# Kernel tuning notes

Measured on AMD Instinct MI355X. Metric: run time of the kernel, lower is better.

The kernel has to match this reference:

```python
import jax, jax.numpy as jnp
import numpy as np

D_MODEL = 1024
D_FF = 4096
EPS = 1e-5


def layer_norm(x, gamma, beta):
    mu = jnp.mean(x, axis=-1, keepdims=True)
    var = jnp.var(x, axis=-1, keepdims=True)
    return (x - mu) * jax.lax.rsqrt(var + EPS) * gamma + beta


def attention(x_q, x_kv, WQ, WK, WV, causal):
    Q = x_q @ WQ          # [B,Sq,D]
    K = x_kv @ WK         # [B,Sk,D]
    V = x_kv @ WV
    scale = 1.0 / jnp.sqrt(jnp.asarray(Q.shape[-1], Q.dtype))
    scores = jnp.einsum('bqd,bkd->bqk', Q, K) * scale
    if causal:
        Sq, Sk = scores.shape[-2], scores.shape[-1]
        mask = jnp.triu(jnp.full((Sq, Sk), -jnp.inf, scores.dtype), k=1)
        scores = scores + mask
    attn = jax.nn.softmax(scores, axis=-1)
    return jnp.einsum('bqk,bkd->bqd', attn, V)


def setup_inputs() -> dict:
    key = jax.random.key(0)
    ks = jax.random.split(key, 16)
    B, S = 4, 2048
    s = 0.02
    inp = {
        'y': jax.random.normal(ks[0], (B, S, D_MODEL), jnp.float32),
        'Z': jax.random.normal(ks[1], (B, S, D_MODEL), jnp.float32),
        'WQ1': jax.random.normal(ks[2], (D_MODEL, D_MODEL), jnp.float32) * s,
        'WK1': jax.random.normal(ks[3], (D_MODEL, D_MODEL), jnp.float32) * s,
        'WV1': jax.random.normal(ks[4], (D_MODEL, D_MODEL), jnp.float32) * s,
        'WQ2': jax.random.normal(ks[5], (D_MODEL, D_MODEL), jnp.float32) * s,
        'WK2': jax.random.normal(ks[6], (D_MODEL, D_MODEL), jnp.float32) * s,
        'WV2': jax.random.normal(ks[7], (D_MODEL, D_MODEL), jnp.float32) * s,
        'W_ff1': jax.random.normal(ks[8], (D_MODEL, D_FF), jnp.float32) * s,
        'b_ff1': jnp.zeros((D_FF,), jnp.float32),
        'W_ff2': jax.random.normal(ks[9], (D_FF, D_MODEL), jnp.float32) * s,
        'b_ff2': jnp.zeros((D_MODEL,), jnp.float32),
        'g1': jnp.ones((D_MODEL,), jnp.float32), 'be1': jnp.zeros((D_MODEL,), jnp.float32),
        'g2': jnp.ones((D_MODEL,), jnp.float32), 'be2': jnp.zeros((D_MODEL,), jnp.float32),
        'g3': jnp.ones((D_MODEL,), jnp.float32), 'be3': jnp.zeros((D_MODEL,), jnp.float32),
    }
    return inp


def reference(y, Z, WQ1, WK1, WV1, WQ2, WK2, WV2, W_ff1, b_ff1, W_ff2, b_ff2,
              g1, be1, g2, be2, g3, be3):
    # masked self-attention + add&norm
    y = layer_norm(y + attention(y, y, WQ1, WK1, WV1, causal=True), g1, be1)
    # cross-attention + add&norm
    y = layer_norm(y + attention(y, Z, WQ2, WK2, WV2, causal=False), g2, be2)
    # FFN + add&norm
    h = jax.nn.relu(y @ W_ff1 + b_ff1) @ W_ff2 + b_ff2
    y = layer_norm(y + h, g3, be3)
    return y
```

## Files before the change

### kernel.cpp

```cpp
#include <hip/hip_runtime.h>
#include <cstddef>

typedef unsigned short u16;
typedef __attribute__((ext_vector_type(8))) short bf16x8;
typedef __attribute__((ext_vector_type(4))) float f32x4;

__device__ __forceinline__ u16 f2bf(float f) {
  union { float f; unsigned u; } x; x.f = f;
  unsigned r = x.u + 0x7fffu + ((x.u >> 16) & 1u);
  return (u16)(r >> 16);
}
__device__ __forceinline__ float bf2f(u16 h) {
  union { unsigned u; float f; } x; x.u = ((unsigned)h) << 16;
  return x.f;
}

__device__ __forceinline__ void gll16(const u16* g, u16* ldsbase) {
  __builtin_amdgcn_global_load_lds(
      (const __attribute__((address_space(1))) void*)g,
      (__attribute__((address_space(3))) void*)ldsbase, 16, 0, 0);
}

__global__ __launch_bounds__(256) void f32_to_bf16(const float* __restrict__ in,
                                                   u16* __restrict__ out, size_t n) {
  size_t i = (size_t)blockIdx.x * 256 + threadIdx.x;
  if (i < n) out[i] = f2bf(in[i]);
}

__global__ __launch_bounds__(256) void transpose_f32_bf16(const float* __restrict__ in,
                                                          u16* __restrict__ out,
                                                          int R, int C) {
  __shared__ float tile[32][33];
  int c0 = blockIdx.x * 32, r0 = blockIdx.y * 32;
  int tx = threadIdx.x & 31, ty = threadIdx.x >> 5;
  #pragma unroll
  for (int i = ty; i < 32; i += 8)
    tile[i][tx] = in[(size_t)(r0 + i) * C + c0 + tx];
  __syncthreads();
  #pragma unroll
  for (int i = ty; i < 32; i += 8)
    out[(size_t)(c0 + i) * R + r0 + tx] = f2bf(tile[tx][i]);
}

enum { EPI_F32 = 0, EPI_BF16 = 1, EPI_BF16_SCALE = 2,
       EPI_BIAS_RELU_BF16 = 3, EPI_BIAS_F32 = 4 };
enum { MODE_FULL = 0, MODE_TRI = 1, MODE_CAUSAL_K = 2 };

template <int EPI, int MODE, int BM, int BN>
__global__ __launch_bounds__(512) void gemm256(
    const u16* __restrict__ A, const u16* __restrict__ Bt,
    void* __restrict__ C0, const float* __restrict__ bias,
    const u16* __restrict__ A2, const u16* __restrict__ B2, int dsplit,
    int K, int lda, int ldb, int ldc,
    long long sA, long long sB, long long sC)
{
  constexpr int WM  = BM / 128;
  constexpr int WN  = 8 / WM;
  constexpr int CPW = BN / WN;
  constexpr int NF  = CPW / 16;
  constexpr int nBr = BN / 64;
  constexpr int nAr = BM / 64;
  constexpr int NBUF = (BM == 256 && BN == 256) ? 2 : 3;

  __shared__ __align__(16) u16 lA[NBUF][BM * 64];
  __shared__ __align__(16) u16 lB[NBUF][BN * 64];

  const unsigned gx = gridDim.x, gxy = gridDim.x * gridDim.y;
  unsigned id = blockIdx.x + gx * blockIdx.y + gxy * blockIdx.z;
  const unsigned nb = gxy * gridDim.z;
  unsigned p = id;
  if ((nb & 7u) == 0u) p = (id & 7u) * (nb >> 3) + (id >> 3);
  int z, mi, ni;
  if constexpr (MODE == MODE_TRI) {
    z = (int)(p / gxy);
    int r = (int)(p % gxy);
    int m = 0;
    if constexpr (BN == 256) {
      while ((m + 1) * (m + 2) / 2 <= r) m++;
      mi = m; ni = r - m * (m + 1) / 2;
    } else {
      while ((m + 1) * (m + 2) <= r) m++;
      mi = m; ni = r - m * (m + 1);
    }
  } else {
    z = (int)(p / gxy);
    const unsigned rem = p % gxy;
    mi = (int)(rem / gx);
    ni = (int)(rem % gx);
  }
  if (dsplit && ni >= dsplit) {
    A = A2; Bt = B2;
    C0 = (void*)((u16*)C0 + (size_t)dsplit * BN);
    ni -= dsplit;
  }
  const int m0 = mi * BM, n0 = ni * BN;

  A  += (long long)z * sA;
  Bt += (long long)z * sB;

  int NT = K >> 6;
  if constexpr (MODE == MODE_CAUSAL_K) NT = (m0 + BM) >> 6;

  const int t    = threadIdx.x;
  const int lane = t & 63;
  const int wave = t >> 6;
  const int wr   = (WM == 1) ? 0 : (wave >> 2);
  const int wc   = (WM == 1) ? wave : (wave & 3);
  const int quad = lane >> 4;
  const int lrow = lane & 15;

  const int srow = lane >> 3;
  const int scol = ((lane & 7) ^ srow) * 8;
  const u16* gAp = A  + (size_t)(m0 + wave * 8 + srow) * lda + scol;
  const u16* gBp = Bt + (size_t)(n0 + wave * 8 + srow) * ldb + scol;
  const size_t a64 = (size_t)64 * lda, b64 = (size_t)64 * ldb;
  const int lw = wave * 512;

  const int pg0 = (quad ^ (lrow & 7)) * 8;
  const int pg1 = pg0 ^ 32;
  const int rA = (wr * 128 + lrow) * 64;
  const int rB = (wc * CPW + lrow) * 64;

  f32x4 acc[8][NF];
  const f32x4 zero = {0.f, 0.f, 0.f, 0.f};
  #pragma unroll
  for (int i = 0; i < 8; i++)
    #pragma unroll
    for (int j = 0; j < NF; j++) acc[i][j] = zero;

  bf16x8 X[4][2];
  bf16x8 Y[4][2];
  bf16x8 bfr[NF][2];

  auto rdX = [&](const u16* s) {
    #pragma unroll
    for (int mf = 0; mf < 4; ++mf) {
      X[mf][0] = *(const bf16x8*)(s + rA + mf * 1024 + pg0);
      X[mf][1] = *(const bf16x8*)(s + rA + mf * 1024 + pg1);
    }
  };
  auto rdY = [&](const u16* s) {
    #pragma unroll
    for (int mf = 0; mf < 4; ++mf) {
      Y[mf][0] = *(const bf16x8*)(s + rA + (mf + 4) * 1024 + pg0);
      Y[mf][1] = *(const bf16x8*)(s + rA + (mf + 4) * 1024 + pg1);
    }
  };
  auto rdB = [&](const u16* s) {
    #pragma unroll
    for (int nf = 0; nf < NF; ++nf) {
      bfr[nf][0] = *(const bf16x8*)(s + rB + nf * 1024 + pg0);
      bfr[nf][1] = *(const bf16x8*)(s + rB + nf * 1024 + pg1);
    }
  };

  if constexpr (NBUF == 2) {
    auto stageB2 = [&](int b, int kt) {
      const int k = kt * 64;
      gll16(gBp + k,           &lB[b][lw]);
      gll16(gBp + k + b64,     &lB[b][4096 + lw]);
      gll16(gBp + k + 2 * b64, &lB[b][8192 + lw]);
      gll16(gBp + k + 3 * b64, &lB[b][12288 + lw]);
    };
    auto stageA2 = [&](int b, int kt) {
      const int k = kt * 64;
      gll16(gAp + k,           &lA[b][lw]);
      gll16(gAp + k + a64,     &lA[b][4096 + lw]);
      gll16(gAp + k + 2 * a64, &lA[b][8192 + lw]);
      gll16(gAp + k + 3 * a64, &lA[b][12288 + lw]);
    };

    stageB2(0, 0); stageA2(0, 0);
    if (NT > 1) {
      stageB2(1, 1);
      asm volatile("s_waitcnt vmcnt(4)" ::: "memory");
    } else {
      asm volatile("s_waitcnt vmcnt(0)" ::: "memory");
    }
    __builtin_amdgcn_s_barrier();

    for (int kt = 0; kt < NT; ++kt) {
      const int bsel = kt & 1;
      const u16* sa = &lA[bsel][0];
      const u16* sb = &lB[bsel][0];

      rdX(sa); rdB(sb);
      if (kt + 1 < NT) stageA2(bsel ^ 1, kt + 1);
      asm volatile("s_waitcnt lgkmcnt(0)" ::: "memory");
      __builtin_amdgcn_sched_barrier(0);
      __builtin_amdgcn_s_setprio(1);
      #pragma unroll
      for (int mf = 0; mf < 4; ++mf)
        #pragma unroll
        for (int nf = 0; nf < 4; ++nf) {
          acc[mf][nf] = __builtin_amdgcn_mfma_f32_16x16x32_bf16(bfr[nf][0], X[mf][0], acc[mf][nf], 0, 0, 0);
          acc[mf][nf] = __builtin_amdgcn_mfma_f32_16x16x32_bf16(bfr[nf][1], X[mf][1], acc[mf][nf], 0, 0, 0);
        }
      __builtin_amdgcn_s_setprio(0);
      __builtin_amdgcn_s_barrier();

      rdY(sa);
      if (kt + 2 < NT) stageB2(bsel, kt + 2);
      asm volatile("s_waitcnt lgkmcnt(0)" ::: "memory");
      __builtin_amdgcn_sched_barrier(0);
      __builtin_amdgcn_s_setprio(1);
      #pragma unroll
      for (int mf = 0; mf < 4; ++mf)
        #pragma unroll
        for (int nf = 0; nf < 4; ++nf) {
          acc[mf + 4][nf] = __builtin_amdgcn_mfma_f32_16x16x32_bf16(bfr[nf][0], Y[mf][0], acc[mf + 4][nf], 0, 0, 0);
          acc[mf + 4][nf] = __builtin_amdgcn_mfma_f32_16x16x32_bf16(bfr[nf][1], Y[mf][1], acc[mf + 4][nf], 0, 0, 0);
        }
      __builtin_amdgcn_s_setprio(0);
      if (kt + 2 < NT)      asm volatile("s_waitcnt vmcnt(4)" ::: "memory");
      else if (kt + 1 < NT) asm volatile("s_waitcnt vmcnt(0)" ::: "memory");
      __builtin_amdgcn_s_barrier();
    }
  } else {
    u16 *a0 = &lA[0][0], *a1 = &lA[1][0], *a2 = &lA[2][0];
    u16 *b0 = &lB[0][0], *b1 = &lB[1][0], *b2 = &lB[2][0];
    auto stage6 = [&](u16* ba, u16* bb, int kt) {
      const int k = kt * 64;
      #pragma unroll
      for (int s = 0; s < nBr; ++s)
        gll16(gBp + k + (size_t)s * b64, bb + s * 4096 + lw);
      #pragma unroll
      for (int s = 0; s < nAr; ++s)
        gll16(gAp + k + (size_t)s * a64, ba + s * 4096 + lw);
    };

    stage6(a0, b0, 0);
    if (NT > 1) {
      stage6(a1, b1, 1);
      asm volatile("s_waitcnt vmcnt(6)" ::: "memory");
    } else {
      asm volatile("s_waitcnt vmcnt(0)" ::: "memory");
    }
    __builtin_amdgcn_s_barrier();

    for (int kt = 0; kt < NT; ++kt) {
      rdX(a0); rdY(a0); rdB(b0);
      if (kt + 2 < NT) stage6(a2, b2, kt + 2);
      asm volatile("s_waitcnt lgkmcnt(0)" ::: "memory");
      __builtin_amdgcn_sched_barrier(0);
      __builtin_amdgcn_s_setprio(1);
      #pragma unroll
      for (int mf = 0; mf < 4; ++mf)
        #pragma unroll
        for (int nf = 0; nf < 2; ++nf) {
          acc[mf][nf] = __builtin_amdgcn_mfma_f32_16x16x32_bf16(bfr[nf][0], X[mf][0], acc[mf][nf], 0, 0, 0);
          acc[mf][nf] = __builtin_amdgcn_mfma_f32_16x16x32_bf16(bfr[nf][1], X[mf][1], acc[mf][nf], 0, 0, 0);
        }
      #pragma unroll
      for (int mf = 0; mf < 4; ++mf)
        #pragma unroll
        for (int nf = 0; nf < 2; ++nf) {
          acc[mf + 4][nf] = __builtin_amdgcn_mfma_f32_16x16x32_bf16(bfr[nf][0], Y[mf][0], acc[mf + 4][nf], 0, 0, 0);
          acc[mf + 4][nf] = __builtin_amdgcn_mfma_f32_16x16x32_bf16(bfr[nf][1], Y[mf][1], acc[mf + 4][nf], 0, 0, 0);
        }
      __builtin_amdgcn_s_setprio(0);
      if (kt + 2 < NT)      asm volatile("s_waitcnt vmcnt(6)" ::: "memory");
      else if (kt + 1 < NT) asm volatile("s_waitcnt vmcnt(0)" ::: "memory");
      __builtin_amdgcn_s_barrier();
      u16* tp;
      tp = a0; a0 = a1; a1 = a2; a2 = tp;
      tp = b0; b0 = b1; b1 = b2; b2 = tp;
    }
  }

  const size_t zoff = (size_t)((long long)z * sC);
  #pragma unroll
  for (int mf = 0; mf < 8; ++mf) {
    #pragma unroll
    for (int nf = 0; nf < NF; ++nf) {
      const size_t m  = (size_t)(m0 + wr * 128 + mf * 16 + lrow);
      const size_t nc = (size_t)(n0 + wc * CPW + nf * 16 + quad * 4);
      const size_t idx = zoff + m * (size_t)ldc + nc;
      f32x4 v = acc[mf][nf];
      if constexpr (EPI == EPI_F32) {
        *(float4*)((float*)C0 + idx) = make_float4(v[0], v[1], v[2], v[3]);
      } else if constexpr (EPI == EPI_BF16) {
        ushort4 o; o.x = f2bf(v[0]); o.y = f2bf(v[1]); o.z = f2bf(v[2]); o.w = f2bf(v[3]);
        *(ushort4*)((u16*)C0 + idx) = o;
      } else if constexpr (EPI == EPI_BF16_SCALE) {
        ushort4 o;
        o.x = f2bf(v[0] * 0.03125f); o.y = f2bf(v[1] * 0.03125f);
        o.z = f2bf(v[2] * 0.03125f); o.w = f2bf(v[3] * 0.03125f);
        *(ushort4*)((u16*)C0 + idx) = o;
      } else if constexpr (EPI == EPI_BIAS_RELU_BF16) {
        const float4 bb = *(const float4*)(bias + nc);
        float y0 = v[0] + bb.x, y1 = v[1] + bb.y, y2 = v[2] + bb.z, y3 = v[3] + bb.w;
        ushort4 o;
        o.x = f2bf(y0 > 0.f ? y0 : 0.f); o.y = f2bf(y1 > 0.f ? y1 : 0.f);
        o.z = f2bf(y2 > 0.f ? y2 : 0.f); o.w = f2bf(y3 > 0.f ? y3 : 0.f);
        *(ushort4*)((u16*)C0 + idx) = o;
      } else {
        const float4 bb = *(const float4*)(bias + nc);
        *(float4*)((float*)C0 + idx) =
            make_float4(v[0] + bb.x, v[1] + bb.y, v[2] + bb.z, v[3] + bb.w);
      }
    }
  }
}

__global__ __launch_bounds__(256) void softmax_bf16(u16* __restrict__ SP, int causal) {
  __shared__ float red[8];
  const int row = blockIdx.x;
  const int q = row & 2047;
  u16* p = SP + (size_t)row * 2048;
  const int t = threadIdx.x;
  const int base = t * 8;
  const int limit  = causal ? (q + 1) : 2048;
  const int wlimit = causal ? (((q >> 8) + 1) << 8) : 2048;

  float v[8];
  if (base < limit) {
    uint4 raw = *(const uint4*)(p + base);
    unsigned w[4] = {raw.x, raw.y, raw.z, raw.w};
    #pragma unroll
    for (int j = 0; j < 4; j++) {
      union { unsigned u; float f; } lo, hi;
      lo.u = w[j] << 16; hi.u = w[j] & 0xffff0000u;
      v[2 * j] = lo.f; v[2 * j + 1] = hi.f;
    }
    #pragma unroll
    for (int j = 0; j < 8; j++) if (base + j >= limit) v[j] = -3.4e38f;
  } else {
    #pragma unroll
    for (int j = 0; j < 8; j++) v[j] = -3.4e38f;
  }

  float mx = v[0];
  #pragma unroll
  for (int j = 1; j < 8; j++) mx = fmaxf(mx, v[j]);
  #pragma unroll
  for (int o = 32; o > 0; o >>= 1) mx = fmaxf(mx, __shfl_down(mx, o));
  if ((t & 63) == 0) red[t >> 6] = mx;
  __syncthreads();
  mx = fmaxf(fmaxf(red[0], red[1]), fmaxf(red[2], red[3]));

  float s = 0.f;
  #pragma unroll
  for (int j = 0; j < 8; j++) { float e = __expf(v[j] - mx); v[j] = e; s += e; }
  #pragma unroll
  for (int o = 32; o > 0; o >>= 1) s += __shfl_down(s, o);
  if ((t & 63) == 0) red[4 + (t >> 6)] = s;
  __syncthreads();
  const float inv = 1.f / (red[4] + red[5] + red[6] + red[7]);

  if (base < wlimit) {
    unsigned o4[4];
    #pragma unroll
    for (int j = 0; j < 4; j++)
      o4[j] = (unsigned)f2bf(v[2 * j] * inv) | ((unsigned)f2bf(v[2 * j + 1] * inv) << 16);
    *(uint4*)(p + base) = make_uint4(o4[0], o4[1], o4[2], o4[3]);
  }
}

template <int ABF>
__global__ __launch_bounds__(256) void ln_residual(const void* __restrict__ a_,
                                                   const float* __restrict__ b,
                                                   const float* __restrict__ g,
                                                   const float* __restrict__ be,
                                                   float* __restrict__ outf,
                                                   u16* __restrict__ outb) {
  __shared__ float red[8];
  const size_t base = (size_t)blockIdx.x * 1024;
  const int t = threadIdx.x;
  const int i0 = t * 4;

  float va[4];
  if constexpr (ABF) {
    const ushort4 h = *(const ushort4*)((const u16*)a_ + base + i0);
    va[0] = bf2f(h.x); va[1] = bf2f(h.y); va[2] = bf2f(h.z); va[3] = bf2f(h.w);
  } else {
    const float4 f = *(const float4*)((const float*)a_ + base + i0);
    va[0] = f.x; va[1] = f.y; va[2] = f.z; va[3] = f.w;
  }
  const float4 vb = *(const float4*)(b + base + i0);
  float v[4] = {va[0] + vb.x, va[1] + vb.y, va[2] + vb.z, va[3] + vb.w};

  float s = v[0] + v[1] + v[2] + v[3];
  #pragma unroll
  for (int o = 32; o > 0; o >>= 1) s += __shfl_down(s, o);
  if ((t & 63) == 0) red[t >> 6] = s;
  __syncthreads();
  const float mean = (red[0] + red[1] + red[2] + red[3]) * (1.f / 1024.f);

  float qq = 0.f;
  #pragma unroll
  for (int i = 0; i < 4; i++) { float d = v[i] - mean; qq += d * d; }
  #pragma unroll
  for (int o = 32; o > 0; o >>= 1) qq += __shfl_down(qq, o);
  if ((t & 63) == 0) red[4 + (t >> 6)] = qq;
  __syncthreads();
  const float rstd = rsqrtf((red[4] + red[5] + red[6] + red[7]) * (1.f / 1024.f) + 1e-5f);

  const float4 gg = *(const float4*)(g + i0);
  const float4 bb = *(const float4*)(be + i0);
  float y0 = (v[0] - mean) * rstd * gg.x + bb.x;
  float y1 = (v[1] - mean) * rstd * gg.y + bb.y;
  float y2 = (v[2] - mean) * rstd * gg.z + bb.z;
  float y3 = (v[3] - mean) * rstd * gg.w + bb.w;
  if (outf) *(float4*)(outf + base + i0) = make_float4(y0, y1, y2, y3);
  if (outb) {
    ushort4 o4; o4.x = f2bf(y0); o4.y = f2bf(y1); o4.z = f2bf(y2); o4.w = f2bf(y3);
    *(ushort4*)(outb + base + i0) = o4;
  }
}

extern "C" void kernel_launch(void* const* d_in, const int* in_sizes, int n_in,
                              void* d_out, int out_size, void* d_ws, size_t ws_size,
                              hipStream_t stream)
{
  const float* y_in = (const float*)d_in[0];
  const float* Z_in = (const float*)d_in[1];
  const float* WQ1  = (const float*)d_in[2];
  const float* WK1  = (const float*)d_in[3];
  const float* WV1  = (const float*)d_in[4];
  const float* WQ2  = (const float*)d_in[5];
  const float* WK2  = (const float*)d_in[6];
  const float* WV2  = (const float*)d_in[7];
  const float* Wff1 = (const float*)d_in[8];
  const float* bff1 = (const float*)d_in[9];
  const float* Wff2 = (const float*)d_in[10];
  const float* bff2 = (const float*)d_in[11];
  const float* g1  = (const float*)d_in[12];
  const float* be1 = (const float*)d_in[13];
  const float* g2  = (const float*)d_in[14];
  const float* be2 = (const float*)d_in[15];
  const float* g3  = (const float*)d_in[16];
  const float* be3 = (const float*)d_in[17];
  (void)in_sizes; (void)n_in; (void)out_size;

  constexpr int Bn = 4, S = 2048, D = 1024, DF = 4096;
  constexpr long long BS = (long long)Bn * S;
  const long long SD = (long long)S * D;
  const long long SS = (long long)S * S;
  const long long SD2 = (long long)S * 2 * D;

  char* ws = (char*)d_ws;
  size_t off = 0;
  auto alloc = [&](size_t bytes) -> char* {
    char* p = ws + off;
    off += (bytes + 255) & ~(size_t)255;
    return p;
  };

  u16* wq1t  = (u16*)alloc((size_t)D * D * 2);
  u16* wk1t  = (u16*)alloc((size_t)D * D * 2);
  u16* wv1t  = (u16*)alloc((size_t)D * D * 2);
  u16* wq2t  = (u16*)alloc((size_t)D * D * 2);
  u16* wk2t  = (u16*)alloc((size_t)D * D * 2);
  u16* wv2t  = (u16*)alloc((size_t)D * D * 2);
  u16* wff1t = (u16*)alloc((size_t)D * DF * 2);
  u16* wff2t = (u16*)alloc((size_t)D * DF * 2);
  u16* ybf   = (u16*)alloc((size_t)BS * D * 2);
  u16* zbf   = (u16*)alloc((size_t)BS * D * 2);
  u16* QKb   = (u16*)alloc((size_t)BS * 2 * D * 2);
  u16* Vtb   = (u16*)alloc((size_t)D * BS * 2);
  u16* SPb   = (u16*)alloc((size_t)Bn * S * S * 2);
  float* attnF = (float*)alloc((size_t)BS * D * 4);
  u16*   y1b = ybf;
  u16*   y2b = zbf;
  u16*   Hb  = QKb;
  float* Fb  = attnF;

  if (off > ws_size) return;

  const dim3 blk(256);
  const dim3 blk512(512);

  f32_to_bf16<<<dim3((unsigned)((BS * D) / 256)), blk, 0, stream>>>(y_in, ybf, (size_t)BS * D);
  f32_to_bf16<<<dim3((unsigned)((BS * D) / 256)), blk, 0, stream>>>(Z_in, zbf, (size_t)BS * D);
  transpose_f32_bf16<<<dim3(D / 32, D / 32), blk, 0, stream>>>(WQ1, wq1t, D, D);
  transpose_f32_bf16<<<dim3(D / 32, D / 32), blk, 0, stream>>>(WK1, wk1t, D, D);
  transpose_f32_bf16<<<dim3(D / 32, D / 32), blk, 0, stream>>>(WV1, wv1t, D, D);
  transpose_f32_bf16<<<dim3(D / 32, D / 32), blk, 0, stream>>>(WQ2, wq2t, D, D);
  transpose_f32_bf16<<<dim3(D / 32, D / 32), blk, 0, stream>>>(WK2, wk2t, D, D);
  transpose_f32_bf16<<<dim3(D / 32, D / 32), blk, 0, stream>>>(WV2, wv2t, D, D);
  transpose_f32_bf16<<<dim3(DF / 32, D / 32), blk, 0, stream>>>(Wff1, wff1t, D, DF);
  transpose_f32_bf16<<<dim3(D / 32, DF / 32), blk, 0, stream>>>(Wff2, wff2t, DF, D);

  gemm256<EPI_BF16, MODE_FULL, 256, 256><<<dim3(2 * D / 256, BS / 256, 1), blk512, 0, stream>>>(
      ybf, wq1t, QKb, nullptr, nullptr, nullptr, 0, D, D, D, 2 * D, 0, 0, 0);
  gemm256<EPI_BF16, MODE_FULL, 128, 256><<<dim3((unsigned)(BS / 256), D / 128, 1), blk512, 0, stream>>>(
      wv1t, ybf, Vtb, nullptr, nullptr, nullptr, 0, D, D, D, (int)BS, 0, 0, 0);
  gemm256<EPI_BF16_SCALE, MODE_TRI, 256, 128><<<dim3(72, 1, Bn), blk512, 0, stream>>>(
      QKb, QKb + D, SPb, nullptr, nullptr, nullptr, 0, D, 2 * D, 2 * D, S, SD2, SD2, SS);
  softmax_bf16<<<dim3((unsigned)(Bn * S)), blk, 0, stream>>>(SPb, 1);
  gemm256<EPI_F32, MODE_CAUSAL_K, 256, 128><<<dim3(D / 128, S / 256, Bn), blk512, 0, stream>>>(
      SPb, Vtb, attnF, nullptr, nullptr, nullptr, 0, S, S, (int)BS, D, SS, S, SD);
  ln_residual<0><<<dim3((unsigned)BS), blk, 0, stream>>>(y_in, attnF, g1, be1, nullptr, y1b);

  gemm256<EPI_BF16, MODE_FULL, 256, 128><<<dim3(2 * D / 128, BS / 256, 1), blk512, 0, stream>>>(
      y1b, wq2t, QKb, nullptr, zbf, wk2t, 8, D, D, D, 2 * D, 0, 0, 0);
  gemm256<EPI_BF16, MODE_FULL, 128, 256><<<dim3((unsigned)(BS / 256), D / 128, 1), blk512, 0, stream>>>(
      wv2t, zbf, Vtb, nullptr, nullptr, nullptr, 0, D, D, D, (int)BS, 0, 0, 0);
  gemm256<EPI_BF16_SCALE, MODE_FULL, 256, 256><<<dim3(S / 256, S / 256, Bn), blk512, 0, stream>>>(
      QKb, QKb + D, SPb, nullptr, nullptr, nullptr, 0, D, 2 * D, 2 * D, S, SD2, SD2, SS);
  softmax_bf16<<<dim3((unsigned)(Bn * S)), blk, 0, stream>>>(SPb, 0);
  gemm256<EPI_F32, MODE_FULL, 256, 128><<<dim3(D / 128, S / 256, Bn), blk512, 0, stream>>>(
      SPb, Vtb, attnF, nullptr, nullptr, nullptr, 0, S, S, (int)BS, D, SS, S, SD);
  ln_residual<1><<<dim3((unsigned)BS), blk, 0, stream>>>(y1b, attnF, g2, be2, nullptr, y2b);

  gemm256<EPI_BIAS_RELU_BF16, MODE_FULL, 256, 256><<<dim3(DF / 256, BS / 256, 1), blk512, 0, stream>>>(
      y2b, wff1t, Hb, bff1, nullptr, nullptr, 0, D, D, D, DF, 0, 0, 0);
  gemm256<EPI_BIAS_F32, MODE_FULL, 256, 128><<<dim3(D / 128, BS / 256, 1), blk512, 0, stream>>>(
      Hb, wff2t, Fb, bff2, nullptr, nullptr, 0, DF, DF, DF, D, 0, 0, 0);
  ln_residual<1><<<dim3((unsigned)BS), blk, 0, stream>>>(y2b, Fb, g3, be3, (float*)d_out, nullptr);
}
```

Measured before the change: 712.9 us.

## Software-pipeline LDS fragment reads with double-buffered registers in GEMM main loop

Restructures both GEMM main loops so the LDS-to-register fragment reads for the next k-tile are issued before the MFMAs of the current tile. Fragments are held in ping-pong register sets (even and odd), and the loop is unrolled by two. Partial lgkmcnt waits replace the full drains, so LDS read latency overlaps matrix-core work. This raises register pressure from the doubled fragment sets, which could cause spills. The new waitcnt and barrier ordering also carries correctness risk.

New measurement: 1.156 ms. 1.62x slower.

```diff
diff --git a/kernel.cpp b/kernel.cpp
--- a/kernel.cpp
+++ b/kernel.cpp
@@ -45,6 +45,93 @@
 enum { EPI_F32 = 0, EPI_BF16 = 1, EPI_BF16_SCALE = 2,
        EPI_BIAS_RELU_BF16 = 3, EPI_BIAS_F32 = 4 };
 enum { MODE_FULL = 0, MODE_TRI = 1, MODE_CAUSAL_K = 2 };
+
+#define RDX(SET, s)                                                           \
+  {                                                                           \
+    _Pragma("unroll")                                                         \
+    for (int mf = 0; mf < 4; ++mf) {                                          \
+      SET[mf][0] = *(const bf16x8*)((s) + rA + mf * 1024 + pg0);              \
+      SET[mf][1] = *(const bf16x8*)((s) + rA + mf * 1024 + pg1);              \
+    }                                                                         \
+  }
+#define RDY(SET, s)                                                           \
+  {                                                                           \
+    _Pragma("unroll")                                                         \
+    for (int mf = 0; mf < 4; ++mf) {                                          \
+      SET[mf][0] = *(const bf16x8*)((s) + rA + (mf + 4) * 1024 + pg0);        \
+      SET[mf][1] = *(const bf16x8*)((s) + rA + (mf + 4) * 1024 + pg1);        \
+    }                                                                         \
+  }
+#define RDBN(SET, s)                                                          \
+  {                                                                           \
+    _Pragma("unroll")                                                         \
+    for (int nf = 0; nf < NF; ++nf) {                                         \
+      SET[nf][0] = *(const bf16x8*)((s) + rB + nf * 1024 + pg0);              \
+      SET[nf][1] = *(const bf16x8*)((s) + rB + nf * 1024 + pg1);              \
+    }                                                                         \
+  }
+#define MMQ(MO, AF, BF)                                                       \
+  {                                                                           \
+    _Pragma("unroll")                                                         \
+    for (int mf = 0; mf < 4; ++mf) {                                          \
+      _Pragma("unroll")                                                       \
+      for (int nf = 0; nf < NF; ++nf) {                                       \
+        acc[mf + MO][nf] = __builtin_amdgcn_mfma_f32_16x16x32_bf16(           \
+            BF[nf][0], AF[mf][0], acc[mf + MO][nf], 0, 0, 0);                 \
+        acc[mf + MO][nf] = __builtin_amdgcn_mfma_f32_16x16x32_bf16(           \
+            BF[nf][1], AF[mf][1], acc[mf + MO][nf], 0, 0, 0);                 \
+      }                                                                       \
+    }                                                                         \
+  }
+
+#define T256(kt, BC, BN_)                                                     \
+  {                                                                           \
+    const int bsel = (kt) & 1;                                                \
+    const u16* sa  = &lA[bsel][0];                                            \
+    const u16* sa1 = &lA[bsel ^ 1][0];                                        \
+    const u16* sb1 = &lB[bsel ^ 1][0];                                        \
+            \
+    RDY(Y, sa);                                                               \
+    if ((kt) + 1 < NT) stageA2(bsel ^ 1, (kt) + 1);                           \
+    __builtin_amdgcn_sched_barrier(0);                                        \
+    asm volatile("s_waitcnt lgkmcnt(8)" ::: "memory");                        \
+    __builtin_amdgcn_sched_barrier(0);                                        \
+    __builtin_amdgcn_s_setprio(1);                                            \
+    MMQ(0, X, BC);                                                            \
+    __builtin_amdgcn_s_setprio(0);                                            \
+    if ((kt) + 1 < NT) asm volatile("s_waitcnt vmcnt(0)" ::: "memory");       \
+    __builtin_amdgcn_s_barrier();                                             \
+        \
+    if ((kt) + 1 < NT) { RDX(X, sa1); RDBN(BN_, sb1); }                       \
+    if ((kt) + 2 < NT) stageB2(bsel, (kt) + 2);                               \
+    __builtin_amdgcn_sched_barrier(0);                                        \
+    if ((kt) + 1 < NT) asm volatile("s_waitcnt lgkmcnt(15)" ::: "memory");    \
+    else               asm volatile("s_waitcnt lgkmcnt(0)" ::: "memory");     \
+    __builtin_amdgcn_sched_barrier(0);                                        \
+    __builtin_amdgcn_s_setprio(1);                                            \
+    MMQ(4, Y, BC);                                                            \
+    __builtin_amdgcn_s_setprio(0);                                            \
+    __builtin_amdgcn_s_barrier();                                             \
+  }
+
+#define TNAR(kt, XC, YC, BC, XN, YN, BN_)                                     \
+  {                                                                           \
+    if ((kt) + 2 < NT) stage6(a2, b2, (kt) + 2);                              \
+    if ((kt) + 1 < NT) { RDX(XN, a1); RDY(YN, a1); RDBN(BN_, b1); }           \
+    __builtin_amdgcn_sched_barrier(0);                                        \
+    if ((kt) + 1 < NT) asm volatile("s_waitcnt lgkmcnt(15)" ::: "memory");    \
+    else               asm volatile("s_waitcnt lgkmcnt(0)" ::: "memory");     \
+    __builtin_amdgcn_sched_barrier(0);                                        \
+    __builtin_amdgcn_s_setprio(1);                                            \
+    MMQ(0, XC, BC);                                                           \
+    MMQ(4, YC, BC);                                                           \
+    __builtin_amdgcn_s_setprio(0);                                            \
+    if ((kt) + 1 < NT) asm volatile("s_waitcnt vmcnt(0)" ::: "memory");       \
+    __builtin_amdgcn_s_barrier();                                             \
+    u16* tp_;                                                                 \
+    tp_ = a0; a0 = a1; a1 = a2; a2 = tp_;                                     \
+    tp_ = b0; b0 = b1; b1 = b2; b2 = tp_;                                     \
+  }
 
 template <int EPI, int MODE, int BM, int BN>
 __global__ __launch_bounds__(512) void gemm256(
@@ -128,33 +215,10 @@
     #pragma unroll
     for (int j = 0; j < NF; j++) acc[i][j] = zero;
 
-  bf16x8 X[4][2];
-  bf16x8 Y[4][2];
-  bf16x8 bfr[NF][2];
-
-  auto rdX = [&](const u16* s) {
-    #pragma unroll
-    for (int mf = 0; mf < 4; ++mf) {
-      X[mf][0] = *(const bf16x8*)(s + rA + mf * 1024 + pg0);
-      X[mf][1] = *(const bf16x8*)(s + rA + mf * 1024 + pg1);
-    }
-  };
-  auto rdY = [&](const u16* s) {
-    #pragma unroll
-    for (int mf = 0; mf < 4; ++mf) {
-      Y[mf][0] = *(const bf16x8*)(s + rA + (mf + 4) * 1024 + pg0);
-      Y[mf][1] = *(const bf16x8*)(s + rA + (mf + 4) * 1024 + pg1);
-    }
-  };
-  auto rdB = [&](const u16* s) {
-    #pragma unroll
-    for (int nf = 0; nf < NF; ++nf) {
-      bfr[nf][0] = *(const bf16x8*)(s + rB + nf * 1024 + pg0);
-      bfr[nf][1] = *(const bf16x8*)(s + rB + nf * 1024 + pg1);
-    }
-  };
-
   if constexpr (NBUF == 2) {
+    bf16x8 X[4][2], Y[4][2];
+    bf16x8 BE[NF][2], BO[NF][2];
+
     auto stageB2 = [&](int b, int kt) {
       const int k = kt * 64;
       gll16(gBp + k,           &lB[b][lw]);
@@ -178,45 +242,16 @@
       asm volatile("s_waitcnt vmcnt(0)" ::: "memory");
     }
     __builtin_amdgcn_s_barrier();
-
-    for (int kt = 0; kt < NT; ++kt) {
-      const int bsel = kt & 1;
-      const u16* sa = &lA[bsel][0];
-      const u16* sb = &lB[bsel][0];
-
-      rdX(sa); rdB(sb);
-      if (kt + 1 < NT) stageA2(bsel ^ 1, kt + 1);
-      asm volatile("s_waitcnt lgkmcnt(0)" ::: "memory");
-      __builtin_amdgcn_sched_barrier(0);
-      __builtin_amdgcn_s_setprio(1);
-      #pragma unroll
-      for (int mf = 0; mf < 4; ++mf)
-        #pragma unroll
-        for (int nf = 0; nf < 4; ++nf) {
-          acc[mf][nf] = __builtin_amdgcn_mfma_f32_16x16x32_bf16(bfr[nf][0], X[mf][0], acc[mf][nf], 0, 0, 0);
-          acc[mf][nf] = __builtin_amdgcn_mfma_f32_16x16x32_bf16(bfr[nf][1], X[mf][1], acc[mf][nf], 0, 0, 0);
-        }
-      __builtin_amdgcn_s_setprio(0);
-      __builtin_amdgcn_s_barrier();
-
-      rdY(sa);
-      if (kt + 2 < NT) stageB2(bsel, kt + 2);
-      asm volatile("s_waitcnt lgkmcnt(0)" ::: "memory");
-      __builtin_amdgcn_sched_barrier(0);
-      __builtin_amdgcn_s_setprio(1);
-      #pragma unroll
-      for (int mf = 0; mf < 4; ++mf)
-        #pragma unroll
-        for (int nf = 0; nf < 4; ++nf) {
-          acc[mf + 4][nf] = __builtin_amdgcn_mfma_f32_16x16x32_bf16(bfr[nf][0], Y[mf][0], acc[mf + 4][nf], 0, 0, 0);
-          acc[mf + 4][nf] = __builtin_amdgcn_mfma_f32_16x16x32_bf16(bfr[nf][1], Y[mf][1], acc[mf + 4][nf], 0, 0, 0);
-        }
-      __builtin_amdgcn_s_setprio(0);
-      if (kt + 2 < NT)      asm volatile("s_waitcnt vmcnt(4)" ::: "memory");
-      else if (kt + 1 < NT) asm volatile("s_waitcnt vmcnt(0)" ::: "memory");
-      __builtin_amdgcn_s_barrier();
+    RDX(X, &lA[0][0]);
+    RDBN(BE, &lB[0][0]);
+
+    for (int kt = 0; kt < NT; kt += 2) {
+      T256(kt, BE, BO);
+      if (kt + 1 < NT) T256(kt + 1, BO, BE);
     }
   } else {
+    bf16x8 XE[4][2], YE[4][2], XO[4][2], YO[4][2];
+    bf16x8 BE[NF][2], BO[NF][2];
     u16 *a0 = &lA[0][0], *a1 = &lA[1][0], *a2 = &lA[2][0];
     u16 *b0 = &lB[0][0], *b1 = &lB[1][0], *b2 = &lB[2][0];
     auto stage6 = [&](u16* ba, u16* bb, int kt) {
@@ -230,41 +265,14 @@
     };
 
     stage6(a0, b0, 0);
-    if (NT > 1) {
-      stage6(a1, b1, 1);
-      asm volatile("s_waitcnt vmcnt(6)" ::: "memory");
-    } else {
-      asm volatile("s_waitcnt vmcnt(0)" ::: "memory");
-    }
+    if (NT > 1) stage6(a1, b1, 1);
+    asm volatile("s_waitcnt vmcnt(0)" ::: "memory");
     __builtin_amdgcn_s_barrier();
-
-    for (int kt = 0; kt < NT; ++kt) {
-      rdX(a0); rdY(a0); rdB(b0);
-      if (kt + 2 < NT) stage6(a2, b2, kt + 2);
-      asm volatile("s_waitcnt lgkmcnt(0)" ::: "memory");
-      __builtin_amdgcn_sched_barrier(0);
-      __builtin_amdgcn_s_setprio(1);
-      #pragma unroll
-      for (int mf = 0; mf < 4; ++mf)
-        #pragma unroll
-        for (int nf = 0; nf < 2; ++nf) {
-          acc[mf][nf] = __builtin_amdgcn_mfma_f32_16x16x32_bf16(bfr[nf][0], X[mf][0], acc[mf][nf], 0, 0, 0);
-          acc[mf][nf] = __builtin_amdgcn_mfma_f32_16x16x32_bf16(bfr[nf][1], X[mf][1], acc[mf][nf], 0, 0, 0);
-        }
-      #pragma unroll
-      for (int mf = 0; mf < 4; ++mf)
-        #pragma unroll
-        for (int nf = 0; nf < 2; ++nf) {
-          acc[mf + 4][nf] = __builtin_amdgcn_mfma_f32_16x16x32_bf16(bfr[nf][0], Y[mf][0], acc[mf + 4][nf], 0, 0, 0);
-          acc[mf + 4][nf] = __builtin_amdgcn_mfma_f32_16x16x32_bf16(bfr[nf][1], Y[mf][1], acc[mf + 4][nf], 0, 0, 0);
-        }
-      __builtin_amdgcn_s_setprio(0);
-      if (kt + 2 < NT)      asm volatile("s_waitcnt vmcnt(6)" ::: "memory");
-      else if (kt + 1 < NT) asm volatile("s_waitcnt vmcnt(0)" ::: "memory");
-      __builtin_amdgcn_s_barrier();
-      u16* tp;
-      tp = a0; a0 = a1; a1 = a2; a2 = tp;
-      tp = b0; b0 = b1; b1 = b2; b2 = tp;
+    RDX(XE, a0); RDY(YE, a0); RDBN(BE, b0);
+
+    for (int kt = 0; kt < NT; kt += 2) {
+      TNAR(kt, XE, YE, BE, XO, YO, BO);
+      if (kt + 1 < NT) TNAR(kt + 1, XO, YO, BO, XE, YE, BE);
     }
   }
 
@@ -303,6 +311,13 @@
   }
 }
 
+#undef T256
+#undef TNAR
+#undef MMQ
+#undef RDX
+#undef RDY
+#undef RDBN
+
 __global__ __launch_bounds__(256) void softmax_bf16(u16* __restrict__ SP, int causal) {
   __shared__ float red[8];
   const int row = blockIdx.x;
```

## Interleave LDS reads, global staging and MFMA in quarter steps; batch weight transposes

Applied to the files above, without the earlier changes.

The 256x256 GEMM main loop is split into four MFMA quarters. Each quarter reads only part of the B fragments from LDS and issues part of the next global-to-LDS staging, so LDS latency and memory traffic overlap with matrix math. The 3-buffer variant changes its wave tiling from 128xCPW to 64x64 and uses graded lgkmcnt waits so MFMA rows start before all fragment reads finish. The six DxD weight transposes become one launch with a z-indexed grid. The extra barriers and finer waits add synchronisation overhead. Merging the transposes assumes the six wq1t..wv2t buffers sit contiguously.

Result: no change. 702.9 us (-1.4%).

```diff
diff --git a/kernel.cpp b/kernel.cpp
--- a/kernel.cpp
+++ b/kernel.cpp
@@ -42,9 +42,60 @@
     out[(size_t)(c0 + i) * R + r0 + tx] = f2bf(tile[tx][i]);
 }
 
+__global__ __launch_bounds__(256) void transpose6_f32_bf16(
+    const float* __restrict__ s0, const float* __restrict__ s1,
+    const float* __restrict__ s2, const float* __restrict__ s3,
+    const float* __restrict__ s4, const float* __restrict__ s5,
+    u16* __restrict__ out) {
+  __shared__ float tile[32][33];
+  const float* srcs[6] = {s0, s1, s2, s3, s4, s5};
+  const float* in = srcs[blockIdx.z];
+  u16* o = out + (size_t)blockIdx.z * 1024 * 1024;
+  int c0 = blockIdx.x * 32, r0 = blockIdx.y * 32;
+  int tx = threadIdx.x & 31, ty = threadIdx.x >> 5;
+  #pragma unroll
+  for (int i = ty; i < 32; i += 8)
+    tile[i][tx] = in[(size_t)(r0 + i) * 1024 + c0 + tx];
+  __syncthreads();
+  #pragma unroll
+  for (int i = ty; i < 32; i += 8)
+    o[(size_t)(c0 + i) * 1024 + r0 + tx] = f2bf(tile[tx][i]);
+}
+
 enum { EPI_F32 = 0, EPI_BF16 = 1, EPI_BF16_SCALE = 2,
        EPI_BIAS_RELU_BF16 = 3, EPI_BIAS_F32 = 4 };
 enum { MODE_FULL = 0, MODE_TRI = 1, MODE_CAUSAL_K = 2 };
+
+#define LGKM(n)                                                               \
+  asm volatile("s_waitcnt lgkmcnt(" #n ")" ::: "memory");                     \
+  __builtin_amdgcn_sched_barrier(0)
+
+#define MMQ16(AF, MO, BF2, NO)                                                \
+  __builtin_amdgcn_s_setprio(1);                                              \
+  _Pragma("unroll")                                                           \
+  for (int mf = 0; mf < 4; ++mf) {                                            \
+    _Pragma("unroll")                                                         \
+    for (int nf = 0; nf < 2; ++nf) {                                          \
+      acc[mf + (MO)][nf + (NO)] = __builtin_amdgcn_mfma_f32_16x16x32_bf16(    \
+          BF2[nf][0], AF[mf][0], acc[mf + (MO)][nf + (NO)], 0, 0, 0);         \
+      acc[mf + (MO)][nf + (NO)] = __builtin_amdgcn_mfma_f32_16x16x32_bf16(    \
+          BF2[nf][1], AF[mf][1], acc[mf + (MO)][nf + (NO)], 0, 0, 0);         \
+    }                                                                         \
+  }                                                                           \
+  __builtin_amdgcn_s_setprio(0);                                              \
+  __builtin_amdgcn_sched_barrier(0)
+
+#define MMROW4(mi)                                                            \
+  __builtin_amdgcn_s_setprio(1);                                              \
+  _Pragma("unroll")                                                           \
+  for (int nf = 0; nf < 4; ++nf) {                                            \
+    acc[mi][nf] = __builtin_amdgcn_mfma_f32_16x16x32_bf16(                    \
+        bfr[nf][0], X[mi][0], acc[mi][nf], 0, 0, 0);                          \
+    acc[mi][nf] = __builtin_amdgcn_mfma_f32_16x16x32_bf16(                    \
+        bfr[nf][1], X[mi][1], acc[mi][nf], 0, 0, 0);                          \
+  }                                                                           \
+  __builtin_amdgcn_s_setprio(0);                                              \
+  __builtin_amdgcn_sched_barrier(0)
 
 template <int EPI, int MODE, int BM, int BN>
 __global__ __launch_bounds__(512) void gemm256(
@@ -54,13 +105,13 @@
     int K, int lda, int ldb, int ldc,
     long long sA, long long sB, long long sC)
 {
-  constexpr int WM  = BM / 128;
-  constexpr int WN  = 8 / WM;
-  constexpr int CPW = BN / WN;
-  constexpr int NF  = CPW / 16;
-  constexpr int nBr = BN / 64;
-  constexpr int nAr = BM / 64;
   constexpr int NBUF = (BM == 256 && BN == 256) ? 2 : 3;
+  constexpr int WTM  = (NBUF == 2) ? 128 : 64;
+  constexpr int WM   = BM / WTM;
+  constexpr int WN   = 8 / WM;
+  constexpr int MF   = WTM / 16;
+  constexpr int nBr  = BN / 64;
+  constexpr int nAr  = BM / 64;
 
   __shared__ __align__(16) u16 lA[NBUF][BM * 64];
   __shared__ __align__(16) u16 lB[NBUF][BN * 64];
@@ -104,8 +155,8 @@
   const int t    = threadIdx.x;
   const int lane = t & 63;
   const int wave = t >> 6;
-  const int wr   = (WM == 1) ? 0 : (wave >> 2);
-  const int wc   = (WM == 1) ? wave : (wave & 3);
+  const int wr   = wave / WN;
+  const int wc   = wave % WN;
   const int quad = lane >> 4;
   const int lrow = lane & 15;
 
@@ -118,62 +169,74 @@
 
   const int pg0 = (quad ^ (lrow & 7)) * 8;
   const int pg1 = pg0 ^ 32;
-  const int rA = (wr * 128 + lrow) * 64;
-  const int rB = (wc * CPW + lrow) * 64;
-
-  f32x4 acc[8][NF];
+  const int rA = (wr * WTM + lrow) * 64;
+  const int rB = (wc * 64 + lrow) * 64;
+
+  f32x4 acc[MF][4];
   const f32x4 zero = {0.f, 0.f, 0.f, 0.f};
   #pragma unroll
-  for (int i = 0; i < 8; i++)
+  for (int i = 0; i < MF; i++)
     #pragma unroll
-    for (int j = 0; j < NF; j++) acc[i][j] = zero;
-
-  bf16x8 X[4][2];
-  bf16x8 Y[4][2];
-  bf16x8 bfr[NF][2];
-
-  auto rdX = [&](const u16* s) {
-    #pragma unroll
-    for (int mf = 0; mf < 4; ++mf) {
-      X[mf][0] = *(const bf16x8*)(s + rA + mf * 1024 + pg0);
-      X[mf][1] = *(const bf16x8*)(s + rA + mf * 1024 + pg1);
-    }
-  };
-  auto rdY = [&](const u16* s) {
-    #pragma unroll
-    for (int mf = 0; mf < 4; ++mf) {
-      Y[mf][0] = *(const bf16x8*)(s + rA + (mf + 4) * 1024 + pg0);
-      Y[mf][1] = *(const bf16x8*)(s + rA + (mf + 4) * 1024 + pg1);
-    }
-  };
-  auto rdB = [&](const u16* s) {
-    #pragma unroll
-    for (int nf = 0; nf < NF; ++nf) {
-      bfr[nf][0] = *(const bf16x8*)(s + rB + nf * 1024 + pg0);
-      bfr[nf][1] = *(const bf16x8*)(s + rB + nf * 1024 + pg1);
-    }
-  };
+    for (int j = 0; j < 4; j++) acc[i][j] = zero;
 
   if constexpr (NBUF == 2) {
-    auto stageB2 = [&](int b, int kt) {
+    bf16x8 X[4][2], Y[4][2];
+    bf16x8 blo[2][2], bhi[2][2];
+
+    auto stAX = [&](int b, int kt) {
+      const int k = kt * 64;
+      gll16(gAp + k,           &lA[b][lw]);
+      gll16(gAp + k + 2 * a64, &lA[b][8192 + lw]);
+    };
+    auto stAY = [&](int b, int kt) {
+      const int k = kt * 64;
+      gll16(gAp + k + a64,     &lA[b][4096 + lw]);
+      gll16(gAp + k + 3 * a64, &lA[b][12288 + lw]);
+    };
+    auto stB01 = [&](int b, int kt) {
       const int k = kt * 64;
       gll16(gBp + k,           &lB[b][lw]);
       gll16(gBp + k + b64,     &lB[b][4096 + lw]);
+    };
+    auto stB23 = [&](int b, int kt) {
+      const int k = kt * 64;
       gll16(gBp + k + 2 * b64, &lB[b][8192 + lw]);
       gll16(gBp + k + 3 * b64, &lB[b][12288 + lw]);
     };
-    auto stageA2 = [&](int b, int kt) {
-      const int k = kt * 64;
-      gll16(gAp + k,           &lA[b][lw]);
-      gll16(gAp + k + a64,     &lA[b][4096 + lw]);
-      gll16(gAp + k + 2 * a64, &lA[b][8192 + lw]);
-      gll16(gAp + k + 3 * a64, &lA[b][12288 + lw]);
-    };
-
-    stageB2(0, 0); stageA2(0, 0);
+
+    auto rdX = [&](const u16* s) {
+      #pragma unroll
+      for (int mf = 0; mf < 4; ++mf) {
+        X[mf][0] = *(const bf16x8*)(s + rA + mf * 1024 + pg0);
+        X[mf][1] = *(const bf16x8*)(s + rA + mf * 1024 + pg1);
+      }
+    };
+    auto rdY = [&](const u16* s) {
+      #pragma unroll
+      for (int mf = 0; mf < 4; ++mf) {
+        Y[mf][0] = *(const bf16x8*)(s + rA + (mf + 4) * 1024 + pg0);
+        Y[mf][1] = *(const bf16x8*)(s + rA + (mf + 4) * 1024 + pg1);
+      }
+    };
+    auto rdBlo = [&](const u16* s) {
+      #pragma unroll
+      for (int nf = 0; nf < 2; ++nf) {
+        blo[nf][0] = *(const bf16x8*)(s + rB + nf * 1024 + pg0);
+        blo[nf][1] = *(const bf16x8*)(s + rB + nf * 1024 + pg1);
+      }
+    };
+    auto rdBhi = [&](const u16* s) {
+      #pragma unroll
+      for (int nf = 0; nf < 2; ++nf) {
+        bhi[nf][0] = *(const bf16x8*)(s + rB + (nf + 2) * 1024 + pg0);
+        bhi[nf][1] = *(const bf16x8*)(s + rB + (nf + 2) * 1024 + pg1);
+      }
+    };
+
+    stAX(0, 0); stB01(0, 0); stB23(0, 0); stAY(0, 0);
     if (NT > 1) {
-      stageB2(1, 1);
-      asm volatile("s_waitcnt vmcnt(4)" ::: "memory");
+      stAX(1, 1); stB01(1, 1); stB23(1, 1);
+      asm volatile("s_waitcnt vmcnt(6)" ::: "memory");
     } else {
       asm volatile("s_waitcnt vmcnt(0)" ::: "memory");
     }
@@ -184,39 +247,41 @@
       const u16* sa = &lA[bsel][0];
       const u16* sb = &lB[bsel][0];
 
-      rdX(sa); rdB(sb);
-      if (kt + 1 < NT) stageA2(bsel ^ 1, kt + 1);
-      asm volatile("s_waitcnt lgkmcnt(0)" ::: "memory");
-      __builtin_amdgcn_sched_barrier(0);
-      __builtin_amdgcn_s_setprio(1);
-      #pragma unroll
-      for (int mf = 0; mf < 4; ++mf)
-        #pragma unroll
-        for (int nf = 0; nf < 4; ++nf) {
-          acc[mf][nf] = __builtin_amdgcn_mfma_f32_16x16x32_bf16(bfr[nf][0], X[mf][0], acc[mf][nf], 0, 0, 0);
-          acc[mf][nf] = __builtin_amdgcn_mfma_f32_16x16x32_bf16(bfr[nf][1], X[mf][1], acc[mf][nf], 0, 0, 0);
-        }
-      __builtin_amdgcn_s_setprio(0);
+      rdX(sa); rdBlo(sb);
+      if (kt + 1 < NT) stAY(bsel ^ 1, kt + 1);
+      asm volatile("s_waitcnt lgkmcnt(8)" ::: "memory");
+      __builtin_amdgcn_s_barrier();
+      LGKM(0);
+      MMQ16(X, 0, blo, 0);
+      __builtin_amdgcn_s_barrier();
+
+      rdBhi(sb);
+      if (kt + 2 < NT) stAX(bsel, kt + 2);
+      __builtin_amdgcn_s_barrier();
+      LGKM(0);
+      MMQ16(X, 0, bhi, 2);
       __builtin_amdgcn_s_barrier();
 
       rdY(sa);
-      if (kt + 2 < NT) stageB2(bsel, kt + 2);
-      asm volatile("s_waitcnt lgkmcnt(0)" ::: "memory");
-      __builtin_amdgcn_sched_barrier(0);
-      __builtin_amdgcn_s_setprio(1);
-      #pragma unroll
-      for (int mf = 0; mf < 4; ++mf)
-        #pragma unroll
-        for (int nf = 0; nf < 4; ++nf) {
-          acc[mf + 4][nf] = __builtin_amdgcn_mfma_f32_16x16x32_bf16(bfr[nf][0], Y[mf][0], acc[mf + 4][nf], 0, 0, 0);
-          acc[mf + 4][nf] = __builtin_amdgcn_mfma_f32_16x16x32_bf16(bfr[nf][1], Y[mf][1], acc[mf + 4][nf], 0, 0, 0);
-        }
-      __builtin_amdgcn_s_setprio(0);
-      if (kt + 2 < NT)      asm volatile("s_waitcnt vmcnt(4)" ::: "memory");
-      else if (kt + 1 < NT) asm volatile("s_waitcnt vmcnt(0)" ::: "memory");
+      if (kt + 2 < NT) stB01(bsel, kt + 2);
+      __builtin_amdgcn_s_barrier();
+      LGKM(0);
+      MMQ16(Y, 4, bhi, 2);
+      __builtin_amdgcn_s_barrier();
+
+      if (kt + 2 < NT) {
+        stB23(bsel, kt + 2);
+        asm volatile("s_waitcnt vmcnt(6)" ::: "memory");
+      } else if (kt + 1 < NT) {
+        asm volatile("s_waitcnt vmcnt(0)" ::: "memory");
+      }
+      __builtin_amdgcn_s_barrier();
+      MMQ16(Y, 4, blo, 0);
       __builtin_amdgcn_s_barrier();
     }
   } else {
+    bf16x8 X[4][2];
+    bf16x8 bfr[4][2];
     u16 *a0 = &lA[0][0], *a1 = &lA[1][0], *a2 = &lA[2][0];
     u16 *b0 = &lB[0][0], *b1 = &lB[1][0], *b2 = &lB[2][0];
     auto stage6 = [&](u16* ba, u16* bb, int kt) {
@@ -227,6 +292,20 @@
       #pragma unroll
       for (int s = 0; s < nAr; ++s)
         gll16(gAp + k + (size_t)s * a64, ba + s * 4096 + lw);
+    };
+    auto rdB4 = [&](const u16* s) {
+      #pragma unroll
+      for (int nf = 0; nf < 4; ++nf) {
+        bfr[nf][0] = *(const bf16x8*)(s + rB + nf * 1024 + pg0);
+        bfr[nf][1] = *(const bf16x8*)(s + rB + nf * 1024 + pg1);
+      }
+    };
+    auto rdX4 = [&](const u16* s) {
+      #pragma unroll
+      for (int mf = 0; mf < 4; ++mf) {
+        X[mf][0] = *(const bf16x8*)(s + rA + mf * 1024 + pg0);
+        X[mf][1] = *(const bf16x8*)(s + rA + mf * 1024 + pg1);
+      }
     };
 
     stage6(a0, b0, 0);
@@ -239,26 +318,12 @@
     __builtin_amdgcn_s_barrier();
 
     for (int kt = 0; kt < NT; ++kt) {
-      rdX(a0); rdY(a0); rdB(b0);
+      rdB4(b0); rdX4(a0);
       if (kt + 2 < NT) stage6(a2, b2, kt + 2);
-      asm volatile("s_waitcnt lgkmcnt(0)" ::: "memory");
-      __builtin_amdgcn_sched_barrier(0);
-      __builtin_amdgcn_s_setprio(1);
-      #pragma unroll
-      for (int mf = 0; mf < 4; ++mf)
-        #pragma unroll
-        for (int nf = 0; nf < 2; ++nf) {
-          acc[mf][nf] = __builtin_amdgcn_mfma_f32_16x16x32_bf16(bfr[nf][0], X[mf][0], acc[mf][nf], 0, 0, 0);
-          acc[mf][nf] = __builtin_amdgcn_mfma_f32_16x16x32_bf16(bfr[nf][1], X[mf][1], acc[mf][nf], 0, 0, 0);
-        }
-      #pragma unroll
-      for (int mf = 0; mf < 4; ++mf)
-        #pragma unroll
-        for (int nf = 0; nf < 2; ++nf) {
-          acc[mf + 4][nf] = __builtin_amdgcn_mfma_f32_16x16x32_bf16(bfr[nf][0], Y[mf][0], acc[mf + 4][nf], 0, 0, 0);
-          acc[mf + 4][nf] = __builtin_amdgcn_mfma_f32_16x16x32_bf16(bfr[nf][1], Y[mf][1], acc[mf + 4][nf], 0, 0, 0);
-        }
-      __builtin_amdgcn_s_setprio(0);
+      LGKM(6);  MMROW4(0);
+      LGKM(4);  MMROW4(1);
+      LGKM(2);  MMROW4(2);
+      LGKM(0);  MMROW4(3);
       if (kt + 2 < NT)      asm volatile("s_waitcnt vmcnt(6)" ::: "memory");
       else if (kt + 1 < NT) asm volatile("s_waitcnt vmcnt(0)" ::: "memory");
       __builtin_amdgcn_s_barrier();
@@ -270,11 +335,11 @@
 
   const size_t zoff = (size_t)((long long)z * sC);
   #pragma unroll
-  for (int mf = 0; mf < 8; ++mf) {
+  for (int mf = 0; mf < MF; ++mf) {
     #pragma unroll
-    for (int nf = 0; nf < NF; ++nf) {
-      const size_t m  = (size_t)(m0 + wr * 128 + mf * 16 + lrow);
-      const size_t nc = (size_t)(n0 + wc * CPW + nf * 16 + quad * 4);
+    for (int nf = 0; nf < 4; ++nf) {
+      const size_t m  = (size_t)(m0 + wr * WTM + mf * 16 + lrow);
+      const size_t nc = (size_t)(n0 + wc * 64 + nf * 16 + quad * 4);
       const size_t idx = zoff + m * (size_t)ldc + nc;
       f32x4 v = acc[mf][nf];
       if constexpr (EPI == EPI_F32) {
@@ -303,6 +368,10 @@
   }
 }
 
+#undef LGKM
+#undef MMQ16
+#undef MMROW4
+
 __global__ __launch_bounds__(256) void softmax_bf16(u16* __restrict__ SP, int causal) {
   __shared__ float red[8];
   const int row = blockIdx.x;
@@ -473,12 +542,8 @@
 
   f32_to_bf16<<<dim3((unsigned)((BS * D) / 256)), blk, 0, stream>>>(y_in, ybf, (size_t)BS * D);
   f32_to_bf16<<<dim3((unsigned)((BS * D) / 256)), blk, 0, stream>>>(Z_in, zbf, (size_t)BS * D);
-  transpose_f32_bf16<<<dim3(D / 32, D / 32), blk, 0, stream>>>(WQ1, wq1t, D, D);
-  transpose_f32_bf16<<<dim3(D / 32, D / 32), blk, 0, stream>>>(WK1, wk1t, D, D);
-  transpose_f32_bf16<<<dim3(D / 32, D / 32), blk, 0, stream>>>(WV1, wv1t, D, D);
-  transpose_f32_bf16<<<dim3(D / 32, D / 32), blk, 0, stream>>>(WQ2, wq2t, D, D);
-  transpose_f32_bf16<<<dim3(D / 32, D / 32), blk, 0, stream>>>(WK2, wk2t, D, D);
-  transpose_f32_bf16<<<dim3(D / 32, D / 32), blk, 0, stream>>>(WV2, wv2t, D, D);
+  transpose6_f32_bf16<<<dim3(D / 32, D / 32, 6), blk, 0, stream>>>(
+      WQ1, WK1, WV1, WQ2, WK2, WV2, wq1t);
   transpose_f32_bf16<<<dim3(DF / 32, D / 32), blk, 0, stream>>>(Wff1, wff1t, D, DF);
   transpose_f32_bf16<<<dim3(D / 32, DF / 32), blk, 0, stream>>>(Wff2, wff2t, DF, D);
 
```
